# Performance work log

Measured on AMD Instinct MI355X. Metric: run time of the kernel, lower is better.

## Reference

```python
import jax, jax.numpy as jnp
import numpy as np

N = 100000
E = 3200000
IN_DIM = 64
HIDDEN = 128
NUM_CLASSES = 10


def setup_inputs() -> dict:
    key = jax.random.key(0)
    ks = jax.random.split(key, 12)
    x = jax.random.normal(ks[0], (N, IN_DIM), dtype=jnp.float32)
    edge_rows = jnp.sort(jax.random.randint(ks[1], (E,), 0, N, dtype=jnp.int32))
    edge_cols = jax.random.randint(ks[2], (E,), 0, N, dtype=jnp.int32)
    edge_vals = jax.random.uniform(ks[3], (E,), dtype=jnp.float32)
    s = 0.05
    fc1_w = jax.random.normal(ks[4], (IN_DIM, HIDDEN), dtype=jnp.float32) * s
    fc1_b = jnp.zeros((HIDDEN,), dtype=jnp.float32)
    fc2_w = jax.random.normal(ks[5], (HIDDEN, HIDDEN), dtype=jnp.float32) * s
    fc2_b = jnp.zeros((HIDDEN,), dtype=jnp.float32)
    att_w = jax.random.normal(ks[6], (HIDDEN, 1), dtype=jnp.float32) * s
    att_b = jnp.zeros((1,), dtype=jnp.float32)
    cls_w = jax.random.normal(ks[7], (HIDDEN, NUM_CLASSES), dtype=jnp.float32) * s
    cls_b = jnp.zeros((NUM_CLASSES,), dtype=jnp.float32)
    return {"x": x, "edge_rows": edge_rows, "edge_cols": edge_cols,
            "edge_vals": edge_vals, "fc1_w": fc1_w, "fc1_b": fc1_b,
            "fc2_w": fc2_w, "fc2_b": fc2_b, "att_w": att_w, "att_b": att_b,
            "cls_w": cls_w, "cls_b": cls_b}


def reference(x, edge_rows, edge_cols, edge_vals,
              fc1_w, fc1_b, fc2_w, fc2_b, att_w, att_b, cls_w, cls_b):
    n = x.shape[0]

    def spmm(mat):  # adj @ mat, adj in COO: out[r] += v * mat[c]
        return jax.ops.segment_sum(edge_vals[:, None] * mat[edge_cols],
                                   edge_rows, num_segments=n)

    h1 = jax.nn.relu(spmm(x @ fc1_w + fc1_b))          # [N, H]
    h2 = jax.nn.relu(spmm(h1 @ fc2_w + fc2_b))         # [N, H]
    h = h1 + h2
    w = jax.nn.softmax(h @ att_w + att_b, axis=0)      # [N, 1] softmax over nodes
    g = jnp.sum(w * h, axis=0)                         # [H]
    return g @ cls_w + cls_b                           # [num_classes]
```

## Files before the change

kernel.cpp:

```cpp
#include <hip/hip_runtime.h>
#include <hip/hip_bf16.h>
#include <math.h>


#define HID 128

__device__ __forceinline__ float relu(float v) { return v > 0.f ? v : 0.f; }

__device__ __forceinline__ unsigned short f2bf(float f) {
  unsigned u = __float_as_uint(f);
  u += 0x7FFFu + ((u >> 16) & 1u);
  return (unsigned short)(u >> 16);
}
__device__ __forceinline__ float bflo(unsigned u) {
  return __uint_as_float(u << 16);
}
__device__ __forceinline__ float bfhi(unsigned u) {
  return __uint_as_float(u & 0xFFFF0000u);
}

__global__ __launch_bounds__(256) void cast_x_kernel(
    const float* __restrict__ x, unsigned short* __restrict__ xb, int n4) {
  int idx = blockIdx.x * 256 + threadIdx.x;
  if (idx < n4) {
    float4 v = *(const float4*)&x[idx * 4];
    ushort4 o;
    o.x = f2bf(v.x); o.y = f2bf(v.y); o.z = f2bf(v.z); o.w = f2bf(v.w);
    *(ushort4*)&xb[idx * 4] = o;
  }
}

__global__ __launch_bounds__(256) void spmm1_kernel(
    const unsigned short* __restrict__ mat, const int* __restrict__ rows,
    const int* __restrict__ cols, const float* __restrict__ vals,
    float* __restrict__ ax, float* __restrict__ rs, int E) {
  int gw0 = (blockIdx.x * blockDim.x + threadIdx.x) >> 6;
  const int gw = __builtin_amdgcn_readfirstlane(gw0);
  const int lane = threadIdx.x & 63;
  const int nw = (gridDim.x * blockDim.x) >> 6;
  const int S = (E + nw - 1) / nw;
  int start = gw * S;
  int end = start + S;
  if (end > E) end = E;
  if (start >= end) return;

  float acc = 0.f, accv = 0.f;
  int curRow = rows[start];

  auto flush = [&]() {
    atomicAdd(ax + (size_t)curRow * 64 + lane, acc);
    if (lane == 0) atomicAdd(rs + curRow, accv);
    acc = 0.f;
    accv = 0.f;
  };

  for (int base = start; base < end; base += 64) {
    const int cnt = min(64, end - base);
    int c_ = 0, r_ = 0;
    float v_ = 0.f;
    if (lane < cnt) {
      int e = base + lane;
      c_ = cols[e];
      v_ = vals[e];
      r_ = rows[e];
    }

    int j = 0;
    for (; j + 8 <= cnt; j += 8) {
      int c0 = __shfl(c_, j + 0), c1 = __shfl(c_, j + 1);
      int c2 = __shfl(c_, j + 2), c3 = __shfl(c_, j + 3);
      int c4 = __shfl(c_, j + 4), c5 = __shfl(c_, j + 5);
      int c6 = __shfl(c_, j + 6), c7 = __shfl(c_, j + 7);
      unsigned u0 = mat[(size_t)c0 * 64 + lane];
      unsigned u1 = mat[(size_t)c1 * 64 + lane];
      unsigned u2 = mat[(size_t)c2 * 64 + lane];
      unsigned u3 = mat[(size_t)c3 * 64 + lane];
      unsigned u4 = mat[(size_t)c4 * 64 + lane];
      unsigned u5 = mat[(size_t)c5 * 64 + lane];
      unsigned u6 = mat[(size_t)c6 * 64 + lane];
      unsigned u7 = mat[(size_t)c7 * 64 + lane];

      float v0 = __shfl(v_, j + 0), v1 = __shfl(v_, j + 1);
      float v2 = __shfl(v_, j + 2), v3 = __shfl(v_, j + 3);
      float v4 = __shfl(v_, j + 4), v5 = __shfl(v_, j + 5);
      float v6 = __shfl(v_, j + 6), v7 = __shfl(v_, j + 7);
      int r0 = __shfl(r_, j + 0), r1 = __shfl(r_, j + 1);
      int r2 = __shfl(r_, j + 2), r3 = __shfl(r_, j + 3);
      int r4 = __shfl(r_, j + 4), r5 = __shfl(r_, j + 5);
      int r6 = __shfl(r_, j + 6), r7 = __shfl(r_, j + 7);

      if (r0 != curRow) { flush(); curRow = r0; }
      acc = fmaf(v0, bflo(u0), acc); accv += v0;
      if (r1 != curRow) { flush(); curRow = r1; }
      acc = fmaf(v1, bflo(u1), acc); accv += v1;
      if (r2 != curRow) { flush(); curRow = r2; }
      acc = fmaf(v2, bflo(u2), acc); accv += v2;
      if (r3 != curRow) { flush(); curRow = r3; }
      acc = fmaf(v3, bflo(u3), acc); accv += v3;
      if (r4 != curRow) { flush(); curRow = r4; }
      acc = fmaf(v4, bflo(u4), acc); accv += v4;
      if (r5 != curRow) { flush(); curRow = r5; }
      acc = fmaf(v5, bflo(u5), acc); accv += v5;
      if (r6 != curRow) { flush(); curRow = r6; }
      acc = fmaf(v6, bflo(u6), acc); accv += v6;
      if (r7 != curRow) { flush(); curRow = r7; }
      acc = fmaf(v7, bflo(u7), acc); accv += v7;
    }
    for (; j < cnt; ++j) {
      int c = __shfl(c_, j);
      float v = __shfl(v_, j);
      int r = __shfl(r_, j);
      if (r != curRow) { flush(); curRow = r; }
      unsigned u = mat[(size_t)c * 64 + lane];
      acc = fmaf(v, bflo(u), acc); accv += v;
    }
  }
  flush();
}

__global__ __launch_bounds__(256) void gemm1_kernel(
    const float* __restrict__ ax, const float* __restrict__ w1,
    const float* __restrict__ b1, const float* __restrict__ rs,
    unsigned short* __restrict__ h1r, int N) {
  __shared__ float w_lds[64 * HID];
  __shared__ float in_lds[64 * 64];
  __shared__ float rs_lds[64];
  const int t = threadIdx.x;
  const int R0 = blockIdx.x * 64;

  for (int idx = t * 4; idx < 64 * HID; idx += 1024)
    *(float4*)&w_lds[idx] = *(const float4*)&w1[idx];
  const int limit = N * 64;
  for (int idx = t * 4; idx < 64 * 64; idx += 1024) {
    int g = R0 * 64 + idx;
    float4 v;
    if (g < limit) v = *(const float4*)&ax[g];
    else { v.x = v.y = v.z = v.w = 0.f; }
    *(float4*)&in_lds[idx] = v;
  }
  if (t < 64) {
    int gr = R0 + t;
    rs_lds[t] = gr < N ? rs[gr] : 0.f;
  }
  __syncthreads();

  const int i = t >> 5, j = t & 31;
  const int r0 = i * 8, c0 = j * 4;
  float4 bv = *(const float4*)&b1[c0];
  float acc[8][4] = {};

#pragma unroll 4
  for (int k = 0; k < 64; ++k) {
    float4 wv = *(const float4*)&w_lds[k * HID + c0];
#pragma unroll
    for (int ii = 0; ii < 8; ++ii) {
      float a = in_lds[(r0 + ii) * 64 + k];
      acc[ii][0] = fmaf(a, wv.x, acc[ii][0]);
      acc[ii][1] = fmaf(a, wv.y, acc[ii][1]);
      acc[ii][2] = fmaf(a, wv.z, acc[ii][2]);
      acc[ii][3] = fmaf(a, wv.w, acc[ii][3]);
    }
  }

#pragma unroll
  for (int ii = 0; ii < 8; ++ii) {
    int gr = R0 + r0 + ii;
    if (gr < N) {
      float rsv = rs_lds[r0 + ii];
      ushort4 o;
      o.x = f2bf(relu(acc[ii][0] + rsv * bv.x));
      o.y = f2bf(relu(acc[ii][1] + rsv * bv.y));
      o.z = f2bf(relu(acc[ii][2] + rsv * bv.z));
      o.w = f2bf(relu(acc[ii][3] + rsv * bv.w));
      *(ushort4*)&h1r[(size_t)gr * HID + c0] = o;
    }
  }
}

__global__ __launch_bounds__(256) void gemm2_kernel(
    const unsigned short* __restrict__ h1r, const float* __restrict__ w2,
    const float* __restrict__ b2, unsigned short* __restrict__ t2, int N) {
  __shared__ unsigned short w_lds[HID * HID];
  __shared__ unsigned short in_lds[64 * HID];
  const int t = threadIdx.x;
  const int R0 = blockIdx.x * 64;

  for (int idx = t * 4; idx < HID * HID; idx += 1024) {
    float4 v = *(const float4*)&w2[idx];
    ushort4 o;
    o.x = f2bf(v.x); o.y = f2bf(v.y); o.z = f2bf(v.z); o.w = f2bf(v.w);
    *(ushort4*)&w_lds[idx] = o;
  }
  const size_t limit = (size_t)N * HID;
  for (int idx = t * 8; idx < 64 * HID; idx += 2048) {
    size_t g = (size_t)R0 * HID + idx;
    uint4 v;
    if (g < limit) v = *(const uint4*)&h1r[g];
    else { v.x = v.y = v.z = v.w = 0u; }
    *(uint4*)&in_lds[idx] = v;
  }
  __syncthreads();

  const int i = t >> 5, j = t & 31;
  const int r0 = i * 8, c0 = j * 4;
  float acc[8][4] = {};

#pragma unroll 2
  for (int k = 0; k < HID; k += 2) {
    ushort4 wu0 = *(const ushort4*)&w_lds[k * HID + c0];
    ushort4 wu1 = *(const ushort4*)&w_lds[(k + 1) * HID + c0];
    float w0x = bflo(wu0.x), w0y = bflo(wu0.y), w0z = bflo(wu0.z), w0w = bflo(wu0.w);
    float w1x = bflo(wu1.x), w1y = bflo(wu1.y), w1z = bflo(wu1.z), w1w = bflo(wu1.w);
#pragma unroll
    for (int ii = 0; ii < 8; ++ii) {
      unsigned au = *(const unsigned*)&in_lds[(r0 + ii) * HID + k];
      float a0 = bflo(au), a1 = bfhi(au);
      acc[ii][0] = fmaf(a1, w1x, fmaf(a0, w0x, acc[ii][0]));
      acc[ii][1] = fmaf(a1, w1y, fmaf(a0, w0y, acc[ii][1]));
      acc[ii][2] = fmaf(a1, w1z, fmaf(a0, w0z, acc[ii][2]));
      acc[ii][3] = fmaf(a1, w1w, fmaf(a0, w0w, acc[ii][3]));
    }
  }

  float4 bv = *(const float4*)&b2[c0];
#pragma unroll
  for (int ii = 0; ii < 8; ++ii) {
    int gr = R0 + r0 + ii;
    if (gr < N) {
      ushort4 o;
      o.x = f2bf(acc[ii][0] + bv.x);
      o.y = f2bf(acc[ii][1] + bv.y);
      o.z = f2bf(acc[ii][2] + bv.z);
      o.w = f2bf(acc[ii][3] + bv.w);
      *(ushort4*)&t2[(size_t)gr * HID + c0] = o;
    }
  }
}

__global__ __launch_bounds__(256) void spmm2_kernel(
    const unsigned short* __restrict__ mat, const int* __restrict__ rows,
    const int* __restrict__ cols, const float* __restrict__ vals,
    float* __restrict__ out, int E) {
  int gw0 = (blockIdx.x * blockDim.x + threadIdx.x) >> 6;
  const int gw = __builtin_amdgcn_readfirstlane(gw0);
  const int lane = threadIdx.x & 63;
  const int nw = (gridDim.x * blockDim.x) >> 6;
  const int S = (E + nw - 1) / nw;
  int start = gw * S;
  int end = start + S;
  if (end > E) end = E;
  if (start >= end) return;

  const int d2 = lane * 2;
  float2 acc = {0.f, 0.f};
  int curRow = rows[start];

  auto flush = [&]() {
    float* o = out + (size_t)curRow * HID + d2;
    atomicAdd(o + 0, acc.x);
    atomicAdd(o + 1, acc.y);
    acc.x = 0.f;
    acc.y = 0.f;
  };

  for (int base = start; base < end; base += 64) {
    const int cnt = min(64, end - base);
    int c_ = 0, r_ = 0;
    float v_ = 0.f;
    if (lane < cnt) {
      int e = base + lane;
      c_ = cols[e];
      v_ = vals[e];
      r_ = rows[e];
    }

    int j = 0;
    for (; j + 4 <= cnt; j += 4) {
      int c0 = __shfl(c_, j + 0), c1 = __shfl(c_, j + 1);
      int c2 = __shfl(c_, j + 2), c3 = __shfl(c_, j + 3);
      float v0 = __shfl(v_, j + 0), v1 = __shfl(v_, j + 1);
      float v2 = __shfl(v_, j + 2), v3 = __shfl(v_, j + 3);
      int r0 = __shfl(r_, j + 0), r1 = __shfl(r_, j + 1);
      int r2 = __shfl(r_, j + 2), r3 = __shfl(r_, j + 3);
      unsigned u0 = *(const unsigned*)(mat + (size_t)c0 * HID + d2);
      unsigned u1 = *(const unsigned*)(mat + (size_t)c1 * HID + d2);
      unsigned u2 = *(const unsigned*)(mat + (size_t)c2 * HID + d2);
      unsigned u3 = *(const unsigned*)(mat + (size_t)c3 * HID + d2);

      if (r0 != curRow) { flush(); curRow = r0; }
      acc.x = fmaf(v0, bflo(u0), acc.x);
      acc.y = fmaf(v0, bfhi(u0), acc.y);
      if (r1 != curRow) { flush(); curRow = r1; }
      acc.x = fmaf(v1, bflo(u1), acc.x);
      acc.y = fmaf(v1, bfhi(u1), acc.y);
      if (r2 != curRow) { flush(); curRow = r2; }
      acc.x = fmaf(v2, bflo(u2), acc.x);
      acc.y = fmaf(v2, bfhi(u2), acc.y);
      if (r3 != curRow) { flush(); curRow = r3; }
      acc.x = fmaf(v3, bflo(u3), acc.x);
      acc.y = fmaf(v3, bfhi(u3), acc.y);
    }
    for (; j < cnt; ++j) {
      int c = __shfl(c_, j);
      float v = __shfl(v_, j);
      int r = __shfl(r_, j);
      if (r != curRow) { flush(); curRow = r; }
      unsigned u = *(const unsigned*)(mat + (size_t)c * HID + d2);
      acc.x = fmaf(v, bflo(u), acc.x);
      acc.y = fmaf(v, bfhi(u), acc.y);
    }
  }
  flush();
}

__global__ __launch_bounds__(256) void att_fused_kernel(
    const unsigned short* __restrict__ h1r, const float* __restrict__ h2p,
    const float* __restrict__ attw, const float* __restrict__ attb,
    float* __restrict__ pm, float* __restrict__ pden,
    float* __restrict__ pnum, int N) {
  __shared__ float sm[4], sden[4], snum[4][HID];
  const int NB = gridDim.x;
  const int w = threadIdx.x >> 6;
  const int lane = threadIdx.x & 63;
  const int gw = blockIdx.x * 4 + w;
  const int nw = NB * 4;
  const float2 wv = *(const float2*)(attw + lane * 2);
  const float b = attb[0];

  float m = -INFINITY, den = 0.f, ax = 0.f, ay = 0.f;
  for (int n = gw; n < N; n += nw) {
    unsigned hu = *(const unsigned*)&h1r[(size_t)n * HID + lane * 2];
    float2 c = *(const float2*)&h2p[(size_t)n * HID + lane * 2];
    float hx = bflo(hu) + relu(c.x);
    float hy = bfhi(hu) + relu(c.y);
    float p = hx * wv.x + hy * wv.y;
#pragma unroll
    for (int off = 1; off < 64; off <<= 1) p += __shfl_xor(p, off);
    float sc = p + b;
    if (sc > m) {
      float scale = expf(m - sc);
      den *= scale; ax *= scale; ay *= scale;
      m = sc;
    }
    float e = expf(sc - m);
    den += e;
    ax = fmaf(e, hx, ax);
    ay = fmaf(e, hy, ay);
  }

  if (lane == 0) { sm[w] = m; sden[w] = den; }
  snum[w][lane * 2] = ax;
  snum[w][lane * 2 + 1] = ay;
  __syncthreads();

  const int t = threadIdx.x;
  if (t < HID) {
    float M4 = fmaxf(fmaxf(sm[0], sm[1]), fmaxf(sm[2], sm[3]));
    float s0 = expf(sm[0] - M4), s1 = expf(sm[1] - M4);
    float s2 = expf(sm[2] - M4), s3 = expf(sm[3] - M4);
    float nv = snum[0][t] * s0 + snum[1][t] * s1 + snum[2][t] * s2 +
               snum[3][t] * s3;
    pnum[(size_t)t * NB + blockIdx.x] = nv;
    if (t == 0) {
      pden[blockIdx.x] = sden[0] * s0 + sden[1] * s1 + sden[2] * s2 +
                         sden[3] * s3;
      pm[blockIdx.x] = M4;
    }
  }
}

__global__ __launch_bounds__(1024) void att_combine_kernel(
    const float* __restrict__ pm, const float* __restrict__ pden,
    const float* __restrict__ pnum, const float* __restrict__ clsw,
    const float* __restrict__ clsb, float* __restrict__ out, int NB) {
  __shared__ float red[1024];
  __shared__ float scale[1024];
  __shared__ float g[HID + 1];
  const int t = threadIdx.x;

  float v = pm[t];
  red[t] = v;
  __syncthreads();
  for (int off = 512; off > 0; off >>= 1) {
    if (t < off) red[t] = fmaxf(red[t], red[t + off]);
    __syncthreads();
  }
  const float M = red[0];
  __syncthreads();

  scale[t] = expf(v - M);
  red[t] = pden[t] * scale[t];
  __syncthreads();
  for (int off = 512; off > 0; off >>= 1) {
    if (t < off) red[t] += red[t + off];
    __syncthreads();
  }
  if (t == 0) g[HID] = red[0];

  const int c = t >> 3, bb = t & 7;
  float acc = 0.f;
  for (int b2 = bb; b2 < NB; b2 += 8) acc += pnum[(size_t)c * NB + b2] * scale[b2];
  acc += __shfl_down(acc, 4);
  acc += __shfl_down(acc, 2);
  acc += __shfl_down(acc, 1);
  if (bb == 0) g[c] = acc;
  __syncthreads();

  if (t < 10) {
    float o = 0.f;
    for (int d = 0; d < HID; ++d) o = fmaf(g[d], clsw[d * 10 + t], o);
    out[t] = clsb[t] + o / g[HID];
  }
}

extern "C" void kernel_launch(void* const* d_in, const int* in_sizes, int n_in,
                              void* d_out, int out_size, void* d_ws,
                              size_t ws_size, hipStream_t stream) {
  const float* x = (const float*)d_in[0];
  const int* erows = (const int*)d_in[1];
  const int* ecols = (const int*)d_in[2];
  const float* evals = (const float*)d_in[3];
  const float* fc1w = (const float*)d_in[4];
  const float* fc1b = (const float*)d_in[5];
  const float* fc2w = (const float*)d_in[6];
  const float* fc2b = (const float*)d_in[7];
  const float* attw = (const float*)d_in[8];
  const float* attb = (const float*)d_in[9];
  const float* clsw = (const float*)d_in[10];
  const float* clsb = (const float*)d_in[11];
  float* out = (float*)d_out;

  const int N = in_sizes[0] / 64;
  const int E = in_sizes[1];
  const int NB = 1024;

  char* base = (char*)d_ws;
  float* ax = (float*)base;
  float* h2p = (float*)(base + (size_t)N * 64 * 4);
  float* rs = (float*)(base + (size_t)N * (64 + 128) * 4);
  unsigned short* xb = (unsigned short*)(base + (size_t)N * (64 + 128 + 1) * 4);
  unsigned short* t2 = (unsigned short*)((char*)xb + (size_t)N * 64 * 2);
  unsigned short* h1r = (unsigned short*)((char*)t2 + (size_t)N * HID * 2);
  float* pm = (float*)((char*)h1r + (size_t)N * HID * 2);
  float* pden = pm + NB;
  float* pnum = pden + NB;

  const int nblk = (N + 63) / 64;

  hipMemsetAsync(ax, 0, (size_t)N * (64 + 128 + 1) * 4, stream);

  cast_x_kernel<<<(N * 64 / 4 + 255) / 256, 256, 0, stream>>>(x, xb, N * 16);
  spmm1_kernel<<<2048, 256, 0, stream>>>(xb, erows, ecols, evals, ax, rs, E);
  gemm1_kernel<<<nblk, 256, 0, stream>>>(ax, fc1w, fc1b, rs, h1r, N);
  gemm2_kernel<<<nblk, 256, 0, stream>>>(h1r, fc2w, fc2b, t2, N);
  spmm2_kernel<<<2048, 256, 0, stream>>>(t2, erows, ecols, evals, h2p, E);
  att_fused_kernel<<<NB, 256, 0, stream>>>(h1r, h2p, attw, attb, pm, pden,
                                           pnum, N);
  att_combine_kernel<<<1, 1024, 0, stream>>>(pm, pden, pnum, clsw, clsb, out,
                                             NB);
}
```

Baseline: 522.9 us.

## Replace SpMM atomics with segmented boundary fixup and fuse SpMM2 with attention

Both SpMM passes now split edges into fixed chunks and write each fully owned row directly. Partial sums for rows that cross a chunk boundary go to side buffers, which a small fixup kernel merges afterwards. This removes the float atomics and the large workspace memset. The second SpMM is fused with the attention softmax pooling, so the fp32 h2 intermediate is never written or re-read, and the combine kernel now reduces over more partial blocks. Nodes with no edges are never written or scored, which only matches the reference when every row has at least one edge; the extra fixup launches are the added cost.

After: 563.5 us. 1.08x slower.

```diff
diff --git a/kernel.cpp b/kernel.cpp
--- a/kernel.cpp
+++ b/kernel.cpp
@@ -4,6 +4,10 @@
 
 
 #define HID 128
+#define NW 8192
+#define NBA 2048
+#define NBC 128
+#define NBT (NBA + NBC)
 
 __device__ __forceinline__ float relu(float v) { return v > 0.f ? v : 0.f; }
 
@@ -33,89 +37,132 @@
 __global__ __launch_bounds__(256) void spmm1_kernel(
     const unsigned short* __restrict__ mat, const int* __restrict__ rows,
     const int* __restrict__ cols, const float* __restrict__ vals,
-    float* __restrict__ ax, float* __restrict__ rs, int E) {
-  int gw0 = (blockIdx.x * blockDim.x + threadIdx.x) >> 6;
-  const int gw = __builtin_amdgcn_readfirstlane(gw0);
+    float* __restrict__ ax, float* __restrict__ rs,
+    int* __restrict__ rowF, int* __restrict__ rowL,
+    float* __restrict__ dataF, float* __restrict__ dataL,
+    float* __restrict__ rsF, float* __restrict__ rsL, int E, int S) {
+  int ch0 = (blockIdx.x * blockDim.x + threadIdx.x) >> 6;
+  const int chunk = __builtin_amdgcn_readfirstlane(ch0);
+  const int lane = threadIdx.x & 63;
+  const int start = chunk * S;
+  const int end = min(start + S, E);
+  int fRow = -1, lRow = -1;
+
+  if (start < end) {
+    const int firstRow = rows[start];
+    const bool cont = (start > 0) && (rows[start - 1] == firstRow);
+    float acc = 0.f, accv = 0.f;
+    int curRow = firstRow;
+
+    auto emit = [&](int nextRow) {
+      if (curRow == firstRow && cont) {
+        dataF[(size_t)chunk * 64 + lane] = acc;
+        if (lane == 0) rsF[chunk] = accv;
+        fRow = curRow;
+      } else {
+        ax[(size_t)curRow * 64 + lane] = acc;
+        if (lane == 0) rs[curRow] = accv;
+      }
+      acc = 0.f; accv = 0.f; curRow = nextRow;
+    };
+
+    for (int base = start; base < end; base += 64) {
+      const int cnt = min(64, end - base);
+      int c_ = 0, r_ = 0;
+      float v_ = 0.f;
+      if (lane < cnt) {
+        int e = base + lane;
+        c_ = cols[e]; v_ = vals[e]; r_ = rows[e];
+      }
+      int j = 0;
+      for (; j + 8 <= cnt; j += 8) {
+        int c0 = __shfl(c_, j + 0), c1 = __shfl(c_, j + 1);
+        int c2 = __shfl(c_, j + 2), c3 = __shfl(c_, j + 3);
+        int c4 = __shfl(c_, j + 4), c5 = __shfl(c_, j + 5);
+        int c6 = __shfl(c_, j + 6), c7 = __shfl(c_, j + 7);
+        unsigned u0 = mat[(size_t)c0 * 64 + lane];
+        unsigned u1 = mat[(size_t)c1 * 64 + lane];
+        unsigned u2 = mat[(size_t)c2 * 64 + lane];
+        unsigned u3 = mat[(size_t)c3 * 64 + lane];
+        unsigned u4 = mat[(size_t)c4 * 64 + lane];
+        unsigned u5 = mat[(size_t)c5 * 64 + lane];
+        unsigned u6 = mat[(size_t)c6 * 64 + lane];
+        unsigned u7 = mat[(size_t)c7 * 64 + lane];
+        float v0 = __shfl(v_, j + 0), v1 = __shfl(v_, j + 1);
+        float v2 = __shfl(v_, j + 2), v3 = __shfl(v_, j + 3);
+        float v4 = __shfl(v_, j + 4), v5 = __shfl(v_, j + 5);
+        float v6 = __shfl(v_, j + 6), v7 = __shfl(v_, j + 7);
+        int r0 = __shfl(r_, j + 0), r1 = __shfl(r_, j + 1);
+        int r2 = __shfl(r_, j + 2), r3 = __shfl(r_, j + 3);
+        int r4 = __shfl(r_, j + 4), r5 = __shfl(r_, j + 5);
+        int r6 = __shfl(r_, j + 6), r7 = __shfl(r_, j + 7);
+
+        if (r0 != curRow) emit(r0);
+        acc = fmaf(v0, bflo(u0), acc); accv += v0;
+        if (r1 != curRow) emit(r1);
+        acc = fmaf(v1, bflo(u1), acc); accv += v1;
+        if (r2 != curRow) emit(r2);
+        acc = fmaf(v2, bflo(u2), acc); accv += v2;
+        if (r3 != curRow) emit(r3);
+        acc = fmaf(v3, bflo(u3), acc); accv += v3;
+        if (r4 != curRow) emit(r4);
+        acc = fmaf(v4, bflo(u4), acc); accv += v4;
+        if (r5 != curRow) emit(r5);
+        acc = fmaf(v5, bflo(u5), acc); accv += v5;
+        if (r6 != curRow) emit(r6);
+        acc = fmaf(v6, bflo(u6), acc); accv += v6;
+        if (r7 != curRow) emit(r7);
+        acc = fmaf(v7, bflo(u7), acc); accv += v7;
+      }
+      for (; j < cnt; ++j) {
+        int c = __shfl(c_, j);
+        float v = __shfl(v_, j);
+        int r = __shfl(r_, j);
+        if (r != curRow) emit(r);
+        unsigned u = mat[(size_t)c * 64 + lane];
+        acc = fmaf(v, bflo(u), acc); accv += v;
+      }
+    }
+    bool spanF = (end < E) && (rows[end] == curRow);
+    if (curRow == firstRow && cont) {
+      dataF[(size_t)chunk * 64 + lane] = acc;
+      if (lane == 0) rsF[chunk] = accv;
+      fRow = curRow;
+    } else if (spanF) {
+      dataL[(size_t)chunk * 64 + lane] = acc;
+      if (lane == 0) rsL[chunk] = accv;
+      lRow = curRow;
+    } else {
+      ax[(size_t)curRow * 64 + lane] = acc;
+      if (lane == 0) rs[curRow] = accv;
+    }
+  }
+  if (lane == 0) { rowF[chunk] = fRow; rowL[chunk] = lRow; }
+}
+
+__global__ __launch_bounds__(256) void spmm1_fix_kernel(
+    const int* __restrict__ rowF, const int* __restrict__ rowL,
+    const float* __restrict__ dataF, const float* __restrict__ dataL,
+    const float* __restrict__ rsF, const float* __restrict__ rsL,
+    float* __restrict__ ax, float* __restrict__ rs) {
+  int wv0 = (blockIdx.x * blockDim.x + threadIdx.x) >> 6;
+  const int gwv = __builtin_amdgcn_readfirstlane(wv0);
   const int lane = threadIdx.x & 63;
   const int nw = (gridDim.x * blockDim.x) >> 6;
-  const int S = (E + nw - 1) / nw;
-  int start = gw * S;
-  int end = start + S;
-  if (end > E) end = E;
-  if (start >= end) return;
-
-  float acc = 0.f, accv = 0.f;
-  int curRow = rows[start];
-
-  auto flush = [&]() {
-    atomicAdd(ax + (size_t)curRow * 64 + lane, acc);
-    if (lane == 0) atomicAdd(rs + curRow, accv);
-    acc = 0.f;
-    accv = 0.f;
-  };
-
-  for (int base = start; base < end; base += 64) {
-    const int cnt = min(64, end - base);
-    int c_ = 0, r_ = 0;
-    float v_ = 0.f;
-    if (lane < cnt) {
-      int e = base + lane;
-      c_ = cols[e];
-      v_ = vals[e];
-      r_ = rows[e];
-    }
-
-    int j = 0;
-    for (; j + 8 <= cnt; j += 8) {
-      int c0 = __shfl(c_, j + 0), c1 = __shfl(c_, j + 1);
-      int c2 = __shfl(c_, j + 2), c3 = __shfl(c_, j + 3);
-      int c4 = __shfl(c_, j + 4), c5 = __shfl(c_, j + 5);
-      int c6 = __shfl(c_, j + 6), c7 = __shfl(c_, j + 7);
-      unsigned u0 = mat[(size_t)c0 * 64 + lane];
-      unsigned u1 = mat[(size_t)c1 * 64 + lane];
-      unsigned u2 = mat[(size_t)c2 * 64 + lane];
-      unsigned u3 = mat[(size_t)c3 * 64 + lane];
-      unsigned u4 = mat[(size_t)c4 * 64 + lane];
-      unsigned u5 = mat[(size_t)c5 * 64 + lane];
-      unsigned u6 = mat[(size_t)c6 * 64 + lane];
-      unsigned u7 = mat[(size_t)c7 * 64 + lane];
-
-      float v0 = __shfl(v_, j + 0), v1 = __shfl(v_, j + 1);
-      float v2 = __shfl(v_, j + 2), v3 = __shfl(v_, j + 3);
-      float v4 = __shfl(v_, j + 4), v5 = __shfl(v_, j + 5);
-      float v6 = __shfl(v_, j + 6), v7 = __shfl(v_, j + 7);
-      int r0 = __shfl(r_, j + 0), r1 = __shfl(r_, j + 1);
-      int r2 = __shfl(r_, j + 2), r3 = __shfl(r_, j + 3);
-      int r4 = __shfl(r_, j + 4), r5 = __shfl(r_, j + 5);
-      int r6 = __shfl(r_, j + 6), r7 = __shfl(r_, j + 7);
-
-      if (r0 != curRow) { flush(); curRow = r0; }
-      acc = fmaf(v0, bflo(u0), acc); accv += v0;
-      if (r1 != curRow) { flush(); curRow = r1; }
-      acc = fmaf(v1, bflo(u1), acc); accv += v1;
-      if (r2 != curRow) { flush(); curRow = r2; }
-      acc = fmaf(v2, bflo(u2), acc); accv += v2;
-      if (r3 != curRow) { flush(); curRow = r3; }
-      acc = fmaf(v3, bflo(u3), acc); accv += v3;
-      if (r4 != curRow) { flush(); curRow = r4; }
-      acc = fmaf(v4, bflo(u4), acc); accv += v4;
-      if (r5 != curRow) { flush(); curRow = r5; }
-      acc = fmaf(v5, bflo(u5), acc); accv += v5;
-      if (r6 != curRow) { flush(); curRow = r6; }
-      acc = fmaf(v6, bflo(u6), acc); accv += v6;
-      if (r7 != curRow) { flush(); curRow = r7; }
-      acc = fmaf(v7, bflo(u7), acc); accv += v7;
-    }
-    for (; j < cnt; ++j) {
-      int c = __shfl(c_, j);
-      float v = __shfl(v_, j);
-      int r = __shfl(r_, j);
-      if (r != curRow) { flush(); curRow = r; }
-      unsigned u = mat[(size_t)c * 64 + lane];
-      acc = fmaf(v, bflo(u), acc); accv += v;
-    }
-  }
-  flush();
+  for (int c = gwv; c < NW; c += nw) {
+    int r = rowL[c];
+    if (r < 0) continue;
+    float acc = dataL[(size_t)c * 64 + lane];
+    float accv = rsL[c];
+    int c2 = c + 1;
+    while (c2 < NW && rowF[c2] == r) {
+      acc += dataF[(size_t)c2 * 64 + lane];
+      accv += rsF[c2];
+      ++c2;
+    }
+    ax[(size_t)r * 64 + lane] = acc;
+    if (lane == 0) rs[r] = accv;
+  }
 }
 
 __global__ __launch_bounds__(256) void gemm1_kernel(
@@ -237,134 +284,203 @@
   }
 }
 
-__global__ __launch_bounds__(256) void spmm2_kernel(
-    const unsigned short* __restrict__ mat, const int* __restrict__ rows,
-    const int* __restrict__ cols, const float* __restrict__ vals,
-    float* __restrict__ out, int E) {
-  int gw0 = (blockIdx.x * blockDim.x + threadIdx.x) >> 6;
-  const int gw = __builtin_amdgcn_readfirstlane(gw0);
-  const int lane = threadIdx.x & 63;
-  const int nw = (gridDim.x * blockDim.x) >> 6;
-  const int S = (E + nw - 1) / nw;
-  int start = gw * S;
-  int end = start + S;
-  if (end > E) end = E;
-  if (start >= end) return;
-
-  const int d2 = lane * 2;
-  float2 acc = {0.f, 0.f};
-  int curRow = rows[start];
-
-  auto flush = [&]() {
-    float* o = out + (size_t)curRow * HID + d2;
-    atomicAdd(o + 0, acc.x);
-    atomicAdd(o + 1, acc.y);
-    acc.x = 0.f;
-    acc.y = 0.f;
-  };
-
-  for (int base = start; base < end; base += 64) {
-    const int cnt = min(64, end - base);
-    int c_ = 0, r_ = 0;
-    float v_ = 0.f;
-    if (lane < cnt) {
-      int e = base + lane;
-      c_ = cols[e];
-      v_ = vals[e];
-      r_ = rows[e];
-    }
-
-    int j = 0;
-    for (; j + 4 <= cnt; j += 4) {
-      int c0 = __shfl(c_, j + 0), c1 = __shfl(c_, j + 1);
-      int c2 = __shfl(c_, j + 2), c3 = __shfl(c_, j + 3);
-      float v0 = __shfl(v_, j + 0), v1 = __shfl(v_, j + 1);
-      float v2 = __shfl(v_, j + 2), v3 = __shfl(v_, j + 3);
-      int r0 = __shfl(r_, j + 0), r1 = __shfl(r_, j + 1);
-      int r2 = __shfl(r_, j + 2), r3 = __shfl(r_, j + 3);
-      unsigned u0 = *(const unsigned*)(mat + (size_t)c0 * HID + d2);
-      unsigned u1 = *(const unsigned*)(mat + (size_t)c1 * HID + d2);
-      unsigned u2 = *(const unsigned*)(mat + (size_t)c2 * HID + d2);
-      unsigned u3 = *(const unsigned*)(mat + (size_t)c3 * HID + d2);
-
-      if (r0 != curRow) { flush(); curRow = r0; }
-      acc.x = fmaf(v0, bflo(u0), acc.x);
-      acc.y = fmaf(v0, bfhi(u0), acc.y);
-      if (r1 != curRow) { flush(); curRow = r1; }
-      acc.x = fmaf(v1, bflo(u1), acc.x);
-      acc.y = fmaf(v1, bfhi(u1), acc.y);
-      if (r2 != curRow) { flush(); curRow = r2; }
-      acc.x = fmaf(v2, bflo(u2), acc.x);
-      acc.y = fmaf(v2, bfhi(u2), acc.y);
-      if (r3 != curRow) { flush(); curRow = r3; }
-      acc.x = fmaf(v3, bflo(u3), acc.x);
-      acc.y = fmaf(v3, bfhi(u3), acc.y);
-    }
-    for (; j < cnt; ++j) {
-      int c = __shfl(c_, j);
-      float v = __shfl(v_, j);
-      int r = __shfl(r_, j);
-      if (r != curRow) { flush(); curRow = r; }
-      unsigned u = *(const unsigned*)(mat + (size_t)c * HID + d2);
-      acc.x = fmaf(v, bflo(u), acc.x);
-      acc.y = fmaf(v, bfhi(u), acc.y);
-    }
-  }
-  flush();
-}
-
-__global__ __launch_bounds__(256) void att_fused_kernel(
-    const unsigned short* __restrict__ h1r, const float* __restrict__ h2p,
-    const float* __restrict__ attw, const float* __restrict__ attb,
-    float* __restrict__ pm, float* __restrict__ pden,
-    float* __restrict__ pnum, int N) {
+__global__ __launch_bounds__(256) void spmm2att_kernel(
+    const unsigned short* __restrict__ mat, const unsigned short* __restrict__ h1r,
+    const int* __restrict__ rows, const int* __restrict__ cols,
+    const float* __restrict__ vals, const float* __restrict__ attw,
+    const float* __restrict__ attb,
+    int* __restrict__ rowF, int* __restrict__ rowL,
+    float* __restrict__ dataF, float* __restrict__ dataL,
+    float* __restrict__ pm, float* __restrict__ pden, float* __restrict__ pnum,
+    int E, int S) {
   __shared__ float sm[4], sden[4], snum[4][HID];
-  const int NB = gridDim.x;
   const int w = threadIdx.x >> 6;
   const int lane = threadIdx.x & 63;
-  const int gw = blockIdx.x * 4 + w;
-  const int nw = NB * 4;
-  const float2 wv = *(const float2*)(attw + lane * 2);
-  const float b = attb[0];
-
-  float m = -INFINITY, den = 0.f, ax = 0.f, ay = 0.f;
-  for (int n = gw; n < N; n += nw) {
-    unsigned hu = *(const unsigned*)&h1r[(size_t)n * HID + lane * 2];
-    float2 c = *(const float2*)&h2p[(size_t)n * HID + lane * 2];
-    float hx = bflo(hu) + relu(c.x);
-    float hy = bfhi(hu) + relu(c.y);
-    float p = hx * wv.x + hy * wv.y;
+  int ch0 = blockIdx.x * 4 + w;
+  const int chunk = __builtin_amdgcn_readfirstlane(ch0);
+  const int start = chunk * S;
+  const int end = min(start + S, E);
+  const int d2 = lane * 2;
+  const float2 wv = *(const float2*)(attw + d2);
+  const float battn = attb[0];
+
+  float m = -INFINITY, den = 0.f, nx = 0.f, ny = 0.f;
+  int fRow = -1, lRow = -1;
+
+  if (start < end) {
+    const int firstRow = rows[start];
+    const bool cont = (start > 0) && (rows[start - 1] == firstRow);
+    float2 acc = {0.f, 0.f};
+    int curRow = firstRow;
+
+    auto attproc = [&](int r, float2 a) {
+      unsigned hu = *(const unsigned*)&h1r[(size_t)r * HID + d2];
+      float hx = bflo(hu) + relu(a.x);
+      float hy = bfhi(hu) + relu(a.y);
+      float p = hx * wv.x + hy * wv.y;
 #pragma unroll
-    for (int off = 1; off < 64; off <<= 1) p += __shfl_xor(p, off);
-    float sc = p + b;
-    if (sc > m) {
-      float scale = expf(m - sc);
-      den *= scale; ax *= scale; ay *= scale;
-      m = sc;
-    }
-    float e = expf(sc - m);
-    den += e;
-    ax = fmaf(e, hx, ax);
-    ay = fmaf(e, hy, ay);
-  }
+      for (int off = 1; off < 64; off <<= 1) p += __shfl_xor(p, off);
+      float sc = p + battn;
+      if (sc > m) {
+        float s = expf(m - sc);
+        den *= s; nx *= s; ny *= s;
+        m = sc;
+      }
+      float e = expf(sc - m);
+      den += e;
+      nx = fmaf(e, hx, nx);
+      ny = fmaf(e, hy, ny);
+    };
+    auto emit = [&](int nextRow) {
+      if (curRow == firstRow && cont) {
+        *(float2*)&dataF[(size_t)chunk * HID + d2] = acc;
+        fRow = curRow;
+      } else {
+        attproc(curRow, acc);
+      }
+      acc.x = acc.y = 0.f;
+      curRow = nextRow;
+    };
+
+    for (int base = start; base < end; base += 64) {
+      const int cnt = min(64, end - base);
+      int c_ = 0, r_ = 0;
+      float v_ = 0.f;
+      if (lane < cnt) {
+        int e = base + lane;
+        c_ = cols[e]; v_ = vals[e]; r_ = rows[e];
+      }
+      int j = 0;
+      for (; j + 4 <= cnt; j += 4) {
+        int c0 = __shfl(c_, j + 0), c1 = __shfl(c_, j + 1);
+        int c2 = __shfl(c_, j + 2), c3 = __shfl(c_, j + 3);
+        float v0 = __shfl(v_, j + 0), v1 = __shfl(v_, j + 1);
+        float v2 = __shfl(v_, j + 2), v3 = __shfl(v_, j + 3);
+        int r0 = __shfl(r_, j + 0), r1 = __shfl(r_, j + 1);
+        int r2 = __shfl(r_, j + 2), r3 = __shfl(r_, j + 3);
+        unsigned u0 = *(const unsigned*)(mat + (size_t)c0 * HID + d2);
+        unsigned u1 = *(const unsigned*)(mat + (size_t)c1 * HID + d2);
+        unsigned u2 = *(const unsigned*)(mat + (size_t)c2 * HID + d2);
+        unsigned u3 = *(const unsigned*)(mat + (size_t)c3 * HID + d2);
+
+        if (r0 != curRow) emit(r0);
+        acc.x = fmaf(v0, bflo(u0), acc.x);
+        acc.y = fmaf(v0, bfhi(u0), acc.y);
+        if (r1 != curRow) emit(r1);
+        acc.x = fmaf(v1, bflo(u1), acc.x);
+        acc.y = fmaf(v1, bfhi(u1), acc.y);
+        if (r2 != curRow) emit(r2);
+        acc.x = fmaf(v2, bflo(u2), acc.x);
+        acc.y = fmaf(v2, bfhi(u2), acc.y);
+        if (r3 != curRow) emit(r3);
+        acc.x = fmaf(v3, bflo(u3), acc.x);
+        acc.y = fmaf(v3, bfhi(u3), acc.y);
+      }
+      for (; j < cnt; ++j) {
+        int c = __shfl(c_, j);
+        float v = __shfl(v_, j);
+        int r = __shfl(r_, j);
+        if (r != curRow) emit(r);
+        unsigned u = *(const unsigned*)(mat + (size_t)c * HID + d2);
+        acc.x = fmaf(v, bflo(u), acc.x);
+        acc.y = fmaf(v, bfhi(u), acc.y);
+      }
+    }
+    bool spanF = (end < E) && (rows[end] == curRow);
+    if (curRow == firstRow && cont) {
+      *(float2*)&dataF[(size_t)chunk * HID + d2] = acc;
+      fRow = curRow;
+    } else if (spanF) {
+      *(float2*)&dataL[(size_t)chunk * HID + d2] = acc;
+      lRow = curRow;
+    } else {
+      attproc(curRow, acc);
+    }
+  }
+  if (lane == 0) { rowF[chunk] = fRow; rowL[chunk] = lRow; }
 
   if (lane == 0) { sm[w] = m; sden[w] = den; }
-  snum[w][lane * 2] = ax;
-  snum[w][lane * 2 + 1] = ay;
-  __syncthreads();
-
+  snum[w][d2] = nx;
+  snum[w][d2 + 1] = ny;
+  __syncthreads();
   const int t = threadIdx.x;
   if (t < HID) {
     float M4 = fmaxf(fmaxf(sm[0], sm[1]), fmaxf(sm[2], sm[3]));
-    float s0 = expf(sm[0] - M4), s1 = expf(sm[1] - M4);
-    float s2 = expf(sm[2] - M4), s3 = expf(sm[3] - M4);
-    float nv = snum[0][t] * s0 + snum[1][t] * s1 + snum[2][t] * s2 +
-               snum[3][t] * s3;
-    pnum[(size_t)t * NB + blockIdx.x] = nv;
+    float s0 = sden[0] > 0.f ? expf(sm[0] - M4) : 0.f;
+    float s1 = sden[1] > 0.f ? expf(sm[1] - M4) : 0.f;
+    float s2 = sden[2] > 0.f ? expf(sm[2] - M4) : 0.f;
+    float s3 = sden[3] > 0.f ? expf(sm[3] - M4) : 0.f;
+    pnum[(size_t)t * NBT + blockIdx.x] =
+        snum[0][t] * s0 + snum[1][t] * s1 + snum[2][t] * s2 + snum[3][t] * s3;
     if (t == 0) {
-      pden[blockIdx.x] = sden[0] * s0 + sden[1] * s1 + sden[2] * s2 +
-                         sden[3] * s3;
+      pden[blockIdx.x] = sden[0] * s0 + sden[1] * s1 + sden[2] * s2 + sden[3] * s3;
       pm[blockIdx.x] = M4;
+    }
+  }
+}
+
+__global__ __launch_bounds__(256) void att_cleanup_kernel(
+    const unsigned short* __restrict__ h1r,
+    const int* __restrict__ rowF, const int* __restrict__ rowL,
+    const float* __restrict__ dataF, const float* __restrict__ dataL,
+    const float* __restrict__ attw, const float* __restrict__ attb,
+    float* __restrict__ pm, float* __restrict__ pden, float* __restrict__ pnum) {
+  __shared__ float sm[4], sden[4], snum[4][HID];
+  const int w = threadIdx.x >> 6;
+  const int lane = threadIdx.x & 63;
+  int wv0 = blockIdx.x * 4 + w;
+  const int gwv = __builtin_amdgcn_readfirstlane(wv0);
+  const int nw = NBC * 4;
+  const int d2 = lane * 2;
+  const float2 wvv = *(const float2*)(attw + d2);
+  const float battn = attb[0];
+
+  float m = -INFINITY, den = 0.f, nx = 0.f, ny = 0.f;
+  for (int c = gwv; c < NW; c += nw) {
+    int r = rowL[c];
+    if (r < 0) continue;
+    float2 acc = *(const float2*)&dataL[(size_t)c * HID + d2];
+    int c2 = c + 1;
+    while (c2 < NW && rowF[c2] == r) {
+      float2 a2 = *(const float2*)&dataF[(size_t)c2 * HID + d2];
+      acc.x += a2.x; acc.y += a2.y;
+      ++c2;
+    }
+    unsigned hu = *(const unsigned*)&h1r[(size_t)r * HID + d2];
+    float hx = bflo(hu) + relu(acc.x);
+    float hy = bfhi(hu) + relu(acc.y);
+    float p = hx * wvv.x + hy * wvv.y;
+#pragma unroll
+    for (int off = 1; off < 64; off <<= 1) p += __shfl_xor(p, off);
+    float sc = p + battn;
+    if (sc > m) {
+      float s = expf(m - sc);
+      den *= s; nx *= s; ny *= s;
+      m = sc;
+    }
+    float e = expf(sc - m);
+    den += e;
+    nx = fmaf(e, hx, nx);
+    ny = fmaf(e, hy, ny);
+  }
+
+  if (lane == 0) { sm[w] = m; sden[w] = den; }
+  snum[w][d2] = nx;
+  snum[w][d2 + 1] = ny;
+  __syncthreads();
+  const int t = threadIdx.x;
+  if (t < HID) {
+    float M4 = fmaxf(fmaxf(sm[0], sm[1]), fmaxf(sm[2], sm[3]));
+    float s0 = sden[0] > 0.f ? expf(sm[0] - M4) : 0.f;
+    float s1 = sden[1] > 0.f ? expf(sm[1] - M4) : 0.f;
+    float s2 = sden[2] > 0.f ? expf(sm[2] - M4) : 0.f;
+    float s3 = sden[3] > 0.f ? expf(sm[3] - M4) : 0.f;
+    int pb = NBA + blockIdx.x;
+    pnum[(size_t)t * NBT + pb] =
+        snum[0][t] * s0 + snum[1][t] * s1 + snum[2][t] * s2 + snum[3][t] * s3;
+    if (t == 0) {
+      pden[pb] = sden[0] * s0 + sden[1] * s1 + sden[2] * s2 + sden[3] * s3;
+      pm[pb] = M4;
     }
   }
 }
@@ -372,14 +488,15 @@
 __global__ __launch_bounds__(1024) void att_combine_kernel(
     const float* __restrict__ pm, const float* __restrict__ pden,
     const float* __restrict__ pnum, const float* __restrict__ clsw,
-    const float* __restrict__ clsb, float* __restrict__ out, int NB) {
+    const float* __restrict__ clsb, float* __restrict__ out) {
   __shared__ float red[1024];
-  __shared__ float scale[1024];
+  __shared__ float scale[NBT];
   __shared__ float g[HID + 1];
   const int t = threadIdx.x;
 
-  float v = pm[t];
-  red[t] = v;
+  float mloc = -INFINITY;
+  for (int i = t; i < NBT; i += 1024) mloc = fmaxf(mloc, pm[i]);
+  red[t] = mloc;
   __syncthreads();
   for (int off = 512; off > 0; off >>= 1) {
     if (t < off) red[t] = fmaxf(red[t], red[t + off]);
@@ -388,18 +505,25 @@
   const float M = red[0];
   __syncthreads();
 
-  scale[t] = expf(v - M);
-  red[t] = pden[t] * scale[t];
+  float dloc = 0.f;
+  for (int i = t; i < NBT; i += 1024) {
+    float dv = pden[i];
+    float sc = dv > 0.f ? expf(pm[i] - M) : 0.f;
+    scale[i] = sc;
+    dloc += dv * sc;
+  }
+  red[t] = dloc;
   __syncthreads();
   for (int off = 512; off > 0; off >>= 1) {
     if (t < off) red[t] += red[t + off];
     __syncthreads();
   }
   if (t == 0) g[HID] = red[0];
+  __syncthreads();
 
   const int c = t >> 3, bb = t & 7;
   float acc = 0.f;
-  for (int b2 = bb; b2 < NB; b2 += 8) acc += pnum[(size_t)c * NB + b2] * scale[b2];
+  for (int i = bb; i < NBT; i += 8) acc += pnum[(size_t)c * NBT + i] * scale[i];
   acc += __shfl_down(acc, 4);
   acc += __shfl_down(acc, 2);
   acc += __shfl_down(acc, 1);
@@ -432,30 +556,49 @@
 
   const int N = in_sizes[0] / 64;
   const int E = in_sizes[1];
-  const int NB = 1024;
-
-  char* base = (char*)d_ws;
-  float* ax = (float*)base;
-  float* h2p = (float*)(base + (size_t)N * 64 * 4);
-  float* rs = (float*)(base + (size_t)N * (64 + 128) * 4);
-  unsigned short* xb = (unsigned short*)(base + (size_t)N * (64 + 128 + 1) * 4);
-  unsigned short* t2 = (unsigned short*)((char*)xb + (size_t)N * 64 * 2);
-  unsigned short* h1r = (unsigned short*)((char*)t2 + (size_t)N * HID * 2);
-  float* pm = (float*)((char*)h1r + (size_t)N * HID * 2);
-  float* pden = pm + NB;
-  float* pnum = pden + NB;
+  const int S = (E + NW - 1) / NW;
+
+  char* p = (char*)d_ws;
+  auto alloc = [&](size_t bytes) {
+    char* q = p;
+    p += (bytes + 255) & ~(size_t)255;
+    return q;
+  };
+  unsigned short* xb = (unsigned short*)alloc((size_t)N * 64 * 2);
+  float* ax = (float*)alloc((size_t)N * 64 * 4);
+  float* rs = (float*)alloc((size_t)N * 4);
+  unsigned short* h1r = (unsigned short*)alloc((size_t)N * HID * 2);
+  unsigned short* t2 = (unsigned short*)alloc((size_t)N * HID * 2);
+  int* rowF1 = (int*)alloc(NW * 4);
+  int* rowL1 = (int*)alloc(NW * 4);
+  float* rsF1 = (float*)alloc(NW * 4);
+  float* rsL1 = (float*)alloc(NW * 4);
+  float* dataF1 = (float*)alloc((size_t)NW * 64 * 4);
+  float* dataL1 = (float*)alloc((size_t)NW * 64 * 4);
+  int* rowF2 = (int*)alloc(NW * 4);
+  int* rowL2 = (int*)alloc(NW * 4);
+  float* dataF2 = (float*)alloc((size_t)NW * HID * 4);
+  float* dataL2 = (float*)alloc((size_t)NW * HID * 4);
+  float* pm = (float*)alloc(NBT * 4);
+  float* pden = (float*)alloc(NBT * 4);
+  float* pnum = (float*)alloc((size_t)HID * NBT * 4);
 
   const int nblk = (N + 63) / 64;
 
-  hipMemsetAsync(ax, 0, (size_t)N * (64 + 128 + 1) * 4, stream);
-
-  cast_x_kernel<<<(N * 64 / 4 + 255) / 256, 256, 0, stream>>>(x, xb, N * 16);
-  spmm1_kernel<<<2048, 256, 0, stream>>>(xb, erows, ecols, evals, ax, rs, E);
+  cast_x_kernel<<<(N * 16 + 255) / 256, 256, 0, stream>>>(x, xb, N * 16);
+  spmm1_kernel<<<NW / 4, 256, 0, stream>>>(xb, erows, ecols, evals, ax, rs,
+                                           rowF1, rowL1, dataF1, dataL1,
+                                           rsF1, rsL1, E, S);
+  spmm1_fix_kernel<<<256, 256, 0, stream>>>(rowF1, rowL1, dataF1, dataL1,
+                                            rsF1, rsL1, ax, rs);
   gemm1_kernel<<<nblk, 256, 0, stream>>>(ax, fc1w, fc1b, rs, h1r, N);
   gemm2_kernel<<<nblk, 256, 0, stream>>>(h1r, fc2w, fc2b, t2, N);
-  spmm2_kernel<<<2048, 256, 0, stream>>>(t2, erows, ecols, evals, h2p, E);
-  att_fused_kernel<<<NB, 256, 0, stream>>>(h1r, h2p, attw, attb, pm, pden,
-                                           pnum, N);
-  att_combine_kernel<<<1, 1024, 0, stream>>>(pm, pden, pnum, clsw, clsb, out,
-                                             NB);
-}
+  spmm2att_kernel<<<NBA, 256, 0, stream>>>(t2, h1r, erows, ecols, evals,
+                                           attw, attb, rowF2, rowL2,
+                                           dataF2, dataL2, pm, pden, pnum,
+                                           E, S);
+  att_cleanup_kernel<<<NBC, 256, 0, stream>>>(h1r, rowF2, rowL2, dataF2,
+                                              dataL2, attw, attb, pm, pden,
+                                              pnum);
+  att_combine_kernel<<<1, 1024, 0, stream>>>(pm, pden, pnum, clsw, clsb, out);
+}
```
